# Kernel optimization log

Hardware: AMD Instinct MI355X
Metric: run time of the kernel (lower is better)

Reference implementation:

```python
import jax, jax.numpy as jnp
import numpy as np
from jax import lax

GEN_POLY = ("1111001", "1011011")  # rate 1/2, constraint length 7 (octal 171/133)


def build_trellis(gen_poly):
    """Feed-forward (non-recursive) convolutional trellis tables.

    State = shift-register contents, most-recent bit is the MSB of the state
    index. Returns int32 tables, each [ns, ni]:
      to_nodes[s, b]        : next state from state s with input bit b
      op_by_fromnode[s, b]  : emitted output-symbol index for (s, b)
      from_nodes[j, m]      : m-th predecessor state of state j
      ip_by_tonode[j, m]    : input bit taken on that predecessor transition
    """
    mu = len(gen_poly[0]) - 1
    ns, ni = 2 ** mu, 2
    g = np.array([[int(c) for c in p] for p in gen_poly])  # [conv_n, mu+1]
    to_nodes = np.zeros((ns, ni), np.int32)
    op_by_fromnode = np.zeros((ns, ni), np.int32)
    from_nodes = np.zeros((ns, ni), np.int32)
    ip_by_tonode = np.zeros((ns, ni), np.int32)
    fill = np.zeros(ns, np.int32)
    for s in range(ns):
        rbits = [(s >> (mu - 1 - j)) & 1 for j in range(mu)]
        for b in range(ni):
            w = np.array([b] + rbits)                 # full window [b, r0..r_{mu-1}]
            obits = (g @ w) % 2                        # output bits, MSB first
            o = int("".join(str(int(x)) for x in obits), 2)
            j = int("".join(str(x) for x in ([b] + rbits[:-1])), 2)
            to_nodes[s, b] = j
            op_by_fromnode[s, b] = o
            from_nodes[j, fill[j]] = s
            ip_by_tonode[j, fill[j]] = b
            fill[j] += 1
    return to_nodes, op_by_fromnode, from_nodes, ip_by_tonode


TO_NODES, OP_BY_FROM, FROM_NODES, IP_BY_TO = build_trellis(GEN_POLY)
CONV_N = len(GEN_POLY)
MU = len(GEN_POLY[0]) - 1
NS = 2 ** MU
NO = 2 ** CONV_N
# output-symbol bit patterns, MSB first, mapped to signs (1-2*bit)
_OP_BITS = np.array([[(o >> (CONV_N - 1 - j)) & 1 for j in range(CONV_N)]
                     for o in range(NO)], np.float32)
OP_SIGN = jnp.asarray(1.0 - 2.0 * _OP_BITS)  # [NO, CONV_N]
IP_SIGN = jnp.asarray([1.0, -1.0])           # sign of input bit b: 1-2b


def setup_inputs() -> dict:
    key = jax.random.key(0)
    k1, k2 = jax.random.split(key)
    B, n = 256, 4096
    T = n // CONV_N  # = k = 2048 info bits
    llr_ch = jax.random.normal(k1, (B, n), dtype=jnp.float32)
    llr_a = jax.random.normal(k2, (B, T), dtype=jnp.float32)
    return {"llr_ch": llr_ch, "llr_a": llr_a}


def _bcjr(llr_ch, llr_a):
    B, n = llr_ch.shape
    T = n // CONV_N
    # branch metrics: bm[t, b, o] = exp(0.5 * sum_j llr[b, t, j] * (1-2*opbit_j(o)))
    llr_r = llr_ch.reshape(B, T, CONV_N)
    bm = jnp.exp(0.5 * jnp.einsum('btj,oj->tbo', llr_r, OP_SIGN))  # [T, B, NO]
    llr_a_t = llr_a.T  # [T, B]

    def gamma_fn(bm_t, la_t):
        # a-priori factor exp(0.5*llr_a*(1-2b)) times channel branch metric
        ap = jnp.exp(0.5 * la_t[:, None, None] * IP_SIGN[None, None, :])  # [B,1,2]
        return ap * bm_t[:, OP_BY_FROM]  # [B, NS, 2]

    alpha0 = jnp.zeros((B, NS), jnp.float32).at[:, 0].set(1.0)

    def fwd(alpha_prev, inp):
        bm_t, la_t = inp
        gam = gamma_fn(bm_t, la_t)                        # [B, NS, 2] by from-state
        ag = gam * alpha_prev[:, :, None]                  # alpha_{t} * gamma_t
        agt = ag[:, FROM_NODES, IP_BY_TO]                  # regroup by to-state
        alpha = agt.sum(-1)
        alpha = alpha / alpha.sum(-1, keepdims=True)       # normalize (as in TF code)
        return alpha, alpha_prev                            # emit alpha BEFORE step t

    _, alphas = lax.scan(fwd, alpha0, (bm, llr_a_t))       # alphas[t] = alpha_t, [T,B,NS]

    beta_T = jnp.full((B, NS), 1.0 / NS, jnp.float32)      # non-terminated: uniform

    def bwd(beta_next, inp):
        bm_t, la_t, alpha_t = inp
        gam = gamma_fn(bm_t, la_t)                         # [B, NS, 2]
        bg = gam * beta_next[:, TO_NODES]                  # gamma * beta_{t+1}(to)
        beta = bg.sum(-1)
        beta = beta / beta.sum(-1, keepdims=True)
        joint = alpha_t[:, :, None] * bg                   # APP per (state, bit)
        llr_t = jnp.log(joint[..., 0].sum(-1)) - jnp.log(joint[..., 1].sum(-1))
        return beta, llr_t

    _, llrs_rev = lax.scan(bwd, beta_T, (bm[::-1], llr_a_t[::-1], alphas[::-1]))
    return llrs_rev[::-1].T  # [B, T] soft LLRs (hard_out=False)


def reference(llr_ch, llr_a):
    return _bcjr(llr_ch, llr_a)
```

## Files before the change

kernel.cpp:

```cpp
#include <hip/hip_runtime.h>

#define T_LEN 2048
#define NSTATE 64
#define NCHUNK 32
#define CH_S 64
#define WARM 64
#define RK 16

template<int CTRL>
__device__ __forceinline__ float dpp_add(float v) {
    int r = __builtin_amdgcn_update_dpp(0, __float_as_int(v), CTRL, 0xF, 0xF, true);
    return v + __int_as_float(r);
}

__device__ __forceinline__ float dpp_sum_to63(float v) {
    v = dpp_add<0x111>(v);
    v = dpp_add<0x112>(v);
    v = dpp_add<0x114>(v);
    v = dpp_add<0x118>(v);
    v = dpp_add<0x142>(v);
    v = dpp_add<0x143>(v);
    return v;
}

__device__ __forceinline__ float wave_total(float v) {
    float s = dpp_sum_to63(v);
    return __int_as_float(__builtin_amdgcn_readlane(__float_as_int(s), 63));
}

__device__ __forceinline__ float pair_sum_xor1(float v) {
    int r = __builtin_amdgcn_update_dpp(0, __float_as_int(v), 0xB1, 0xF, 0xF, true);
    return v + __int_as_float(r);
}

__device__ __forceinline__ unsigned short bf16_of(float f) {
    return (unsigned short)((__float_as_uint(f) + 0x8000u) >> 16);
}


__global__ __launch_bounds__(256, 8)
void bcjr_fwd_kernel(const float* __restrict__ llr_ch,
                     const float* __restrict__ llr_a,
                     unsigned short* __restrict__ wsA)
{
    const int wave  = blockIdx.x * 4 + (threadIdx.x >> 6);
    const int lane  = threadIdx.x & 63;
    const int chunk = wave & (NCHUNK - 1);
    const int b     = wave >> 5;

    const float c0 = 1.0f - 2.0f * (float)(__popc(lane & 57) & 1);
    const float c1 = 1.0f - 2.0f * (float)(__popc(lane & 27) & 1);
    const float kE = 0.5f * 1.442695040888963f;
    const float k0 = kE * c0, k1 = kE * c1;

    const float* chp = llr_ch + (size_t)b * (2 * T_LEN);
    const float* lap = llr_a  + (size_t)b * T_LEN;
    unsigned short* w = wsA + (size_t)b * T_LEN * NSTATE;

    const int  fs0 = 2 * (lane & 31);
    const bool fhi = (lane >= 32);
    const int t0 = chunk * CH_S;
    const int ts = (chunk == 0) ? t0 : t0 - WARM;
    float state = (chunk == 0) ? ((lane == 0) ? 1.0f : 0.0f) : (1.0f / 64.0f);

    for (int g = ts; g < t0 + CH_S; g += RK) {
        const bool store = (g >= t0);
        #pragma unroll
        for (int h = 0; h < 2; ++h) {
            const int gb = g + 8 * h;
            const float4* c4 = (const float4*)(chp + 2 * gb);
            const float4* a4 = (const float4*)(lap + gb);
            float4 cc[4], aa[2];
            #pragma unroll
            for (int i = 0; i < 4; ++i) cc[i] = c4[i];
            #pragma unroll
            for (int i = 0; i < 2; ++i) aa[i] = a4[i];
            unsigned short* wb = w + (size_t)gb * NSTATE + lane;
            #pragma unroll
            for (int i = 0; i < 8; ++i) {
                float l0 = (i & 1) ? cc[i >> 1].z : cc[i >> 1].x;
                float l1 = (i & 1) ? cc[i >> 1].w : cc[i >> 1].y;
                float la = ((const float*)aa)[i];
                if (store) wb[i * NSTATE] = bf16_of(state);
                float x   = fmaf(la, kE, fmaf(l0, k0, l1 * k1));
                float g0v = exp2f(x);
                float g1v = __builtin_amdgcn_rcpf(g0v);
                float s0  = pair_sum_xor1(state * g0v);
                float s1  = pair_sum_xor1(state * g1v);
                float a0  = __shfl(s0, fs0, 64);
                float a1  = __shfl(s1, fs0, 64);
                state = fhi ? a1 : a0;
            }
        }
        float s = wave_total(state);
        state = state * __builtin_amdgcn_rcpf(s);
    }
}

__global__ __launch_bounds__(256, 8)
void bcjr_bwd_llr_kernel(const float* __restrict__ llr_ch,
                         const float* __restrict__ llr_a,
                         const unsigned short* __restrict__ wsA,
                         float* __restrict__ out)
{
    const int wave  = blockIdx.x * 4 + (threadIdx.x >> 6);
    const int lane  = threadIdx.x & 63;
    const int chunk = wave & (NCHUNK - 1);
    const int b     = wave >> 5;

    const float c0 = 1.0f - 2.0f * (float)(__popc(lane & 57) & 1);
    const float c1 = 1.0f - 2.0f * (float)(__popc(lane & 27) & 1);
    const float kE = 0.5f * 1.442695040888963f;
    const float k0 = kE * c0, k1 = kE * c1;

    const float* chp = llr_ch + (size_t)b * (2 * T_LEN);
    const float* lap = llr_a  + (size_t)b * T_LEN;
    const unsigned short* wa = wsA + (size_t)b * T_LEN * NSTATE;
    float* outp = out + (size_t)b * T_LEN;

    const int  bs0 = lane >> 1;
    const int  bs1 = 32 + (lane >> 1);
    const int t0 = chunk * CH_S;
    const int te = (chunk == NCHUNK - 1) ? (t0 + CH_S) : (t0 + CH_S + WARM);
    float state = 1.0f / 64.0f;

    for (int g = te - RK; g >= t0; g -= RK) {
        const bool act = (g < t0 + CH_S);
        #pragma unroll
        for (int h = 1; h >= 0; --h) {
            const int gb = g + 8 * h;
            const float4* c4 = (const float4*)(chp + 2 * gb);
            const float4* a4 = (const float4*)(lap + gb);
            float4 cc[4], aa[2];
            #pragma unroll
            for (int i = 0; i < 4; ++i) cc[i] = c4[i];
            #pragma unroll
            for (int i = 0; i < 2; ++i) aa[i] = a4[i];
            float av[8];
            if (act) {
                const unsigned short* ap = wa + (size_t)gb * NSTATE + lane;
                #pragma unroll
                for (int i = 0; i < 8; ++i)
                    av[i] = __uint_as_float(((unsigned)ap[i * NSTATE]) << 16);
            }
            #pragma unroll
            for (int i = 7; i >= 0; --i) {
                float l0 = (i & 1) ? cc[i >> 1].z : cc[i >> 1].x;
                float l1 = (i & 1) ? cc[i >> 1].w : cc[i >> 1].y;
                float la = ((const float*)aa)[i];
                float x   = fmaf(la, kE, fmaf(l0, k0, l1 * k1));
                float g0v = exp2f(x);
                float g1v = __builtin_amdgcn_rcpf(g0v);
                float t0v = __shfl(state, bs0, 64);
                float t1v = __shfl(state, bs1, 64);
                float p0 = g0v * t0v;
                float p1 = g1v * t1v;
                if (act) {
                    float na = dpp_sum_to63(av[i] * p0);
                    float nb = dpp_sum_to63(av[i] * p1);
                    float d  = (__log2f(na) - __log2f(nb)) * 0.6931471805599453f;
                    if (lane == 63) outp[gb + i] = d;
                }
                state = p0 + p1;
            }
        }
        float s = wave_total(state);
        state = state * __builtin_amdgcn_rcpf(s);
    }
}

extern "C" void kernel_launch(void* const* d_in, const int* in_sizes, int n_in,
                              void* d_out, int out_size, void* d_ws, size_t ws_size,
                              hipStream_t stream) {
    const float* llr_ch = (const float*)d_in[0];
    const float* llr_a  = (const float*)d_in[1];
    float* out = (float*)d_out;

    int B = in_sizes[0] / (2 * T_LEN);
    unsigned short* wsA = (unsigned short*)d_ws;

    int n_waves = B * NCHUNK;
    hipLaunchKernelGGL(bcjr_fwd_kernel, dim3(n_waves / 4), dim3(256), 0, stream,
                       llr_ch, llr_a, wsA);
    hipLaunchKernelGGL(bcjr_bwd_llr_kernel, dim3(n_waves / 4), dim3(256), 0, stream,
                       llr_ch, llr_a, wsA, out);
}
```

Measured before the change: 151.0 us.

## Fuse forward and backward BCJR passes into one kernel with alphas in LDS

Merges the two kernels into one. Each block has one forward wave and one backward wave working on the same chunk. The forward wave writes its bf16 alphas to shared memory instead of a global workspace. The backward wave runs its warm-up at the same time, then waits at a barrier and reads the alphas from LDS to compute LLRs. This removes the global alpha round-trip and one kernel launch, and overlaps the two warm-up recursions. The cost is a serialization point: the backward LLR phase cannot start until the whole forward chunk is done, and blocks are smaller.

```diff
diff --git a/kernel.cpp b/kernel.cpp
--- a/kernel.cpp
+++ b/kernel.cpp
@@ -38,15 +38,108 @@
 }
 
 
-__global__ __launch_bounds__(256, 8)
-void bcjr_fwd_kernel(const float* __restrict__ llr_ch,
-                     const float* __restrict__ llr_a,
-                     unsigned short* __restrict__ wsA)
+template<bool STORE>
+__device__ __forceinline__ float fwd_group(float state,
+                                           const float* __restrict__ chp,
+                                           const float* __restrict__ lap,
+                                           unsigned short* __restrict__ alds,
+                                           int g, int t0, int lane,
+                                           float kE, float k0, float k1,
+                                           int fs0, bool fhi)
 {
-    const int wave  = blockIdx.x * 4 + (threadIdx.x >> 6);
+    #pragma unroll
+    for (int h = 0; h < 2; ++h) {
+        const int gb = g + 8 * h;
+        const float4* c4 = (const float4*)(chp + 2 * gb);
+        const float4* a4 = (const float4*)(lap + gb);
+        float4 cc[4], aa[2];
+        #pragma unroll
+        for (int i = 0; i < 4; ++i) cc[i] = c4[i];
+        #pragma unroll
+        for (int i = 0; i < 2; ++i) aa[i] = a4[i];
+        #pragma unroll
+        for (int i = 0; i < 8; ++i) {
+            float l0 = (i & 1) ? cc[i >> 1].z : cc[i >> 1].x;
+            float l1 = (i & 1) ? cc[i >> 1].w : cc[i >> 1].y;
+            float la = ((const float*)aa)[i];
+            if (STORE) alds[(gb + i - t0) * NSTATE + lane] = bf16_of(state);
+            float x   = fmaf(la, kE, fmaf(l0, k0, l1 * k1));
+            float g0v = exp2f(x);
+            float g1v = __builtin_amdgcn_rcpf(g0v);
+            float s0  = pair_sum_xor1(state * g0v);
+            float s1  = pair_sum_xor1(state * g1v);
+            float a0  = __shfl(s0, fs0, 64);
+            float a1  = __shfl(s1, fs0, 64);
+            state = fhi ? a1 : a0;
+        }
+    }
+    float s = wave_total(state);
+    return state * __builtin_amdgcn_rcpf(s);
+}
+
+template<bool LLR>
+__device__ __forceinline__ float bwd_group(float state,
+                                           const float* __restrict__ chp,
+                                           const float* __restrict__ lap,
+                                           const unsigned short* __restrict__ alds,
+                                           float* __restrict__ outp,
+                                           int g, int t0, int lane,
+                                           float kE, float k0, float k1,
+                                           int bs0, int bs1)
+{
+    #pragma unroll
+    for (int h = 1; h >= 0; --h) {
+        const int gb = g + 8 * h;
+        const float4* c4 = (const float4*)(chp + 2 * gb);
+        const float4* a4 = (const float4*)(lap + gb);
+        float4 cc[4], aa[2];
+        #pragma unroll
+        for (int i = 0; i < 4; ++i) cc[i] = c4[i];
+        #pragma unroll
+        for (int i = 0; i < 2; ++i) aa[i] = a4[i];
+        float av[8];
+        if (LLR) {
+            #pragma unroll
+            for (int i = 0; i < 8; ++i)
+                av[i] = __uint_as_float(((unsigned)alds[(gb + i - t0) * NSTATE + lane]) << 16);
+        }
+        #pragma unroll
+        for (int i = 7; i >= 0; --i) {
+            float l0 = (i & 1) ? cc[i >> 1].z : cc[i >> 1].x;
+            float l1 = (i & 1) ? cc[i >> 1].w : cc[i >> 1].y;
+            float la = ((const float*)aa)[i];
+            float x   = fmaf(la, kE, fmaf(l0, k0, l1 * k1));
+            float g0v = exp2f(x);
+            float g1v = __builtin_amdgcn_rcpf(g0v);
+            float t0v = __shfl(state, bs0, 64);
+            float t1v = __shfl(state, bs1, 64);
+            float p0 = g0v * t0v;
+            float p1 = g1v * t1v;
+            if (LLR) {
+                float na = dpp_sum_to63(av[i] * p0);
+                float nb = dpp_sum_to63(av[i] * p1);
+                float d  = (__log2f(na) - __log2f(nb)) * 0.6931471805599453f;
+                if (lane == 63) outp[gb + i] = d;
+            }
+            state = p0 + p1;
+        }
+    }
+    float s = wave_total(state);
+    return state * __builtin_amdgcn_rcpf(s);
+}
+
+__global__ __launch_bounds__(128, 8)
+void bcjr_fused_kernel(const float* __restrict__ llr_ch,
+                       const float* __restrict__ llr_a,
+                       float* __restrict__ out)
+{
+    __shared__ unsigned short alds[CH_S * NSTATE];
+
     const int lane  = threadIdx.x & 63;
-    const int chunk = wave & (NCHUNK - 1);
-    const int b     = wave >> 5;
+    const int role  = threadIdx.x >> 6;
+    const int unit  = blockIdx.x;
+    const int chunk = unit & (NCHUNK - 1);
+    const int b     = unit >> 5;
 
     const float c0 = 1.0f - 2.0f * (float)(__popc(lane & 57) & 1);
     const float c1 = 1.0f - 2.0f * (float)(__popc(lane & 27) & 1);
@@ -55,117 +148,29 @@
 
     const float* chp = llr_ch + (size_t)b * (2 * T_LEN);
     const float* lap = llr_a  + (size_t)b * T_LEN;
-    unsigned short* w = wsA + (size_t)b * T_LEN * NSTATE;
+    const int t0 = chunk * CH_S;
 
-    const int  fs0 = 2 * (lane & 31);
-    const bool fhi = (lane >= 32);
-    const int t0 = chunk * CH_S;
-    const int ts = (chunk == 0) ? t0 : t0 - WARM;
-    float state = (chunk == 0) ? ((lane == 0) ? 1.0f : 0.0f) : (1.0f / 64.0f);
-
-    for (int g = ts; g < t0 + CH_S; g += RK) {
-        const bool store = (g >= t0);
-        #pragma unroll
-        for (int h = 0; h < 2; ++h) {
-            const int gb = g + 8 * h;
-            const float4* c4 = (const float4*)(chp + 2 * gb);
-            const float4* a4 = (const float4*)(lap + gb);
-            float4 cc[4], aa[2];
-            #pragma unroll
-            for (int i = 0; i < 4; ++i) cc[i] = c4[i];
-            #pragma unroll
-            for (int i = 0; i < 2; ++i) aa[i] = a4[i];
-            unsigned short* wb = w + (size_t)gb * NSTATE + lane;
-            #pragma unroll
-            for (int i = 0; i < 8; ++i) {
-                float l0 = (i & 1) ? cc[i >> 1].z : cc[i >> 1].x;
-                float l1 = (i & 1) ? cc[i >> 1].w : cc[i >> 1].y;
-                float la = ((const float*)aa)[i];
-                if (store) wb[i * NSTATE] = bf16_of(state);
-                float x   = fmaf(la, kE, fmaf(l0, k0, l1 * k1));
-                float g0v = exp2f(x);
-                float g1v = __builtin_amdgcn_rcpf(g0v);
-                float s0  = pair_sum_xor1(state * g0v);
-                float s1  = pair_sum_xor1(state * g1v);
-                float a0  = __shfl(s0, fs0, 64);
-                float a1  = __shfl(s1, fs0, 64);
-                state = fhi ? a1 : a0;
-            }
-        }
-        float s = wave_total(state);
-        state = state * __builtin_amdgcn_rcpf(s);
-    }
-}
-
-__global__ __launch_bounds__(256, 8)
-void bcjr_bwd_llr_kernel(const float* __restrict__ llr_ch,
-                         const float* __restrict__ llr_a,
-                         const unsigned short* __restrict__ wsA,
-                         float* __restrict__ out)
-{
-    const int wave  = blockIdx.x * 4 + (threadIdx.x >> 6);
-    const int lane  = threadIdx.x & 63;
-    const int chunk = wave & (NCHUNK - 1);
-    const int b     = wave >> 5;
-
-    const float c0 = 1.0f - 2.0f * (float)(__popc(lane & 57) & 1);
-    const float c1 = 1.0f - 2.0f * (float)(__popc(lane & 27) & 1);
-    const float kE = 0.5f * 1.442695040888963f;
-    const float k0 = kE * c0, k1 = kE * c1;
-
-    const float* chp = llr_ch + (size_t)b * (2 * T_LEN);
-    const float* lap = llr_a  + (size_t)b * T_LEN;
-    const unsigned short* wa = wsA + (size_t)b * T_LEN * NSTATE;
-    float* outp = out + (size_t)b * T_LEN;
-
-    const int  bs0 = lane >> 1;
-    const int  bs1 = 32 + (lane >> 1);
-    const int t0 = chunk * CH_S;
-    const int te = (chunk == NCHUNK - 1) ? (t0 + CH_S) : (t0 + CH_S + WARM);
-    float state = 1.0f / 64.0f;
-
-    for (int g = te - RK; g >= t0; g -= RK) {
-        const bool act = (g < t0 + CH_S);
-        #pragma unroll
-        for (int h = 1; h >= 0; --h) {
-            const int gb = g + 8 * h;
-            const float4* c4 = (const float4*)(chp + 2 * gb);
-            const float4* a4 = (const float4*)(lap + gb);
-            float4 cc[4], aa[2];
-            #pragma unroll
-            for (int i = 0; i < 4; ++i) cc[i] = c4[i];
-            #pragma unroll
-            for (int i = 0; i < 2; ++i) aa[i] = a4[i];
-            float av[8];
-            if (act) {
-                const unsigned short* ap = wa + (size_t)gb * NSTATE + lane;
-                #pragma unroll
-                for (int i = 0; i < 8; ++i)
-                    av[i] = __uint_as_float(((unsigned)ap[i * NSTATE]) << 16);
-            }
-            #pragma unroll
-            for (int i = 7; i >= 0; --i) {
-                float l0 = (i & 1) ? cc[i >> 1].z : cc[i >> 1].x;
-                float l1 = (i & 1) ? cc[i >> 1].w : cc[i >> 1].y;
-                float la = ((const float*)aa)[i];
-                float x   = fmaf(la, kE, fmaf(l0, k0, l1 * k1));
-                float g0v = exp2f(x);
-                float g1v = __builtin_amdgcn_rcpf(g0v);
-                float t0v = __shfl(state, bs0, 64);
-                float t1v = __shfl(state, bs1, 64);
-                float p0 = g0v * t0v;
-                float p1 = g1v * t1v;
-                if (act) {
-                    float na = dpp_sum_to63(av[i] * p0);
-                    float nb = dpp_sum_to63(av[i] * p1);
-                    float d  = (__log2f(na) - __log2f(nb)) * 0.6931471805599453f;
-                    if (lane == 63) outp[gb + i] = d;
-                }
-                state = p0 + p1;
-            }
-        }
-        float s = wave_total(state);
-        state = state * __builtin_amdgcn_rcpf(s);
+    if (role == 0) {
+        const int  fs0 = 2 * (lane & 31);
+        const bool fhi = (lane >= 32);
+        float state = (chunk == 0) ? ((lane == 0) ? 1.0f : 0.0f) : (1.0f / 64.0f);
+        const int ts = (chunk == 0) ? t0 : t0 - WARM;
+        for (int g = ts; g < t0; g += RK)
+            state = fwd_group<false>(state, chp, lap, alds, g, t0, lane, kE, k0, k1, fs0, fhi);
+        for (int g = t0; g < t0 + CH_S; g += RK)
+            state = fwd_group<true>(state, chp, lap, alds, g, t0, lane, kE, k0, k1, fs0, fhi);
+        __syncthreads();
+    } else {
+        const int bs0 = lane >> 1;
+        const int bs1 = 32 + (lane >> 1);
+        float state = 1.0f / 64.0f;
+        const int te = (chunk == NCHUNK - 1) ? (t0 + CH_S) : (t0 + CH_S + WARM);
+        for (int g = te - RK; g >= t0 + CH_S; g -= RK)
+            state = bwd_group<false>(state, chp, lap, alds, nullptr, g, t0, lane, kE, k0, k1, bs0, bs1);
+        __syncthreads();
+        float* outp = out + (size_t)b * T_LEN;
+        for (int g = t0 + CH_S - RK; g >= t0; g -= RK)
+            state = bwd_group<true>(state, chp, lap, alds, outp, g, t0, lane, kE, k0, k1, bs0, bs1);
     }
 }
 
@@ -177,11 +182,9 @@
     float* out = (float*)d_out;
 
     int B = in_sizes[0] / (2 * T_LEN);
-    unsigned short* wsA = (unsigned short*)d_ws;
+    (void)d_ws; (void)ws_size;
 
-    int n_waves = B * NCHUNK;
-    hipLaunchKernelGGL(bcjr_fwd_kernel, dim3(n_waves / 4), dim3(256), 0, stream,
-                       llr_ch, llr_a, wsA);
-    hipLaunchKernelGGL(bcjr_bwd_llr_kernel, dim3(n_waves / 4), dim3(256), 0, stream,
-                       llr_ch, llr_a, wsA, out);
+    int n_units = B * NCHUNK;
+    hipLaunchKernelGGL(bcjr_fused_kernel, dim3(n_units), dim3(128), 0, stream,
+                       llr_ch, llr_a, out);
 }
```

Result: faster. 141.4 us (-6.4%).
